# Kernel optimization log

Hardware: AMD Instinct MI355X
Metric: run time of the kernel (lower is better)

The kernel has to match this reference:

```python
import jax, jax.numpy as jnp
import numpy as np

N_ATOMS = 16384
M_NBR = 32  # neighbors per center


def setup_inputs() -> dict:
    key = jax.random.key(0)
    k1, k2, k3 = jax.random.split(key, 3)
    # atom positions in a 10 A box so a realistic fraction of pairs fall inside cutoffs
    coords = jax.random.uniform(k1, (N_ATOMS, 3), jnp.float32) * 10.0
    centers = jnp.arange(N_ATOMS, dtype=jnp.int32)
    # neighbors distinct from the center: center + offset in [1, N) mod N
    off = jax.random.randint(k2, (N_ATOMS, M_NBR), 1, N_ATOMS, dtype=jnp.int32)
    nbrs = (centers[:, None] + off) % N_ATOMS
    nl = jnp.concatenate([centers[:, None], nbrs], axis=1)  # [N, M+1]
    elements = jax.random.randint(k3, (N_ATOMS, M_NBR + 1), 0, 2, dtype=jnp.int32)
    # Stillinger-Weber parameters from __init__ (indexed by elem-sum)
    A = jnp.array([3.9781804791, 11.3797414404, 1.1907355764], jnp.float32)
    B = jnp.array([0.4446021306, 0.5266688197, 0.9015152673], jnp.float32)
    p = jnp.array([5.0, 5.0, 5.0], jnp.float32)
    q = jnp.array([0.0, 0.0, 0.0], jnp.float32)
    sigma = jnp.array([2.85295, 2.17517, 2.84133], jnp.float32)
    gamma = jnp.array([1.3566322033, 1.3566322033, 1.3566322033], jnp.float32)
    cutoff = jnp.array([5.5466, 4.02692, 4.51956], jnp.float32)
    lam = jnp.array([7.4767529158, 8.159518122], jnp.float32)
    cos_beta0 = jnp.array([0.1428569579923222, 0.1428569579923222], jnp.float32)
    cutoff_jk = jnp.array([3.86095, 5.5466], jnp.float32)
    return dict(coords=coords, A=A, B=B, p=p, q=q, sigma=sigma, gamma=gamma,
                cutoff=cutoff, lam=lam, cos_beta0=cos_beta0, cutoff_jk=cutoff_jk,
                elements=elements, nl=nl)


def reference(coords, A, B, p, q, sigma, gamma, cutoff, lam, cos_beta0, cutoff_jk, elements, nl):
    ci = nl[:, 0]            # [N] center atom indices
    nj = nl[:, 1:]           # [N, M] neighbor indices
    xi = coords[ci][:, None, :]       # [N,1,3]
    dij = coords[nj] - xi             # [N,M,3]
    rij = jnp.sqrt(jnp.sum(dij * dij, -1))  # [N,M]
    ei = elements[:, 0:1]             # [N,1]
    ej = elements[:, 1:]              # [N,M]

    # ---- two-body term ----
    s2 = ei + ej                      # in {0,1,2}
    A2, B2, p2, q2 = A[s2], B[s2], p[s2], q[s2]
    sg2, c2 = sigma[s2], cutoff[s2]
    m2 = rij < c2
    r2 = jnp.where(m2, rij, 0.5 * c2)  # safe value for masked lanes
    sr = sg2 / r2
    E2 = A2 * (B2 * sr ** p2 - sr ** q2) * jnp.exp(sg2 / (r2 - c2))
    e_pair = 0.5 * jnp.sum(jnp.where(m2, E2, 0.0))

    # ---- three-body term over all j<k neighbor pairs per center ----
    Mn = rij.shape[1]
    jj, kk = np.triu_indices(Mn, 1)   # static triplet enumeration, T = M(M-1)/2
    rij_t, rik_t = rij[:, jj], rij[:, kk]            # [N,T]
    djk = dij[:, kk, :] - dij[:, jj, :]
    rjk_t = jnp.sqrt(jnp.sum(djk * djk, -1))
    ej_t, ek_t = ej[:, jj], ej[:, kk]
    cond = (ei != ej_t) & (ej_t == ek_t)
    ijk = jnp.clip(2 - (ei + ej_t + ek_t), 0, 1)     # index into 2-entry lists
    gij, cij = gamma[ei + ej_t], cutoff[ei + ej_t]
    gik, cik = gamma[ei + ek_t], cutoff[ei + ek_t]
    cjk = cutoff_jk[ijk]
    m3 = cond & (rij_t < cij) & (rik_t < cik) & (rjk_t < cjk)
    rij_s = jnp.where(rij_t < cij, rij_t, 0.5 * cij)
    rik_s = jnp.where(rik_t < cik, rik_t, 0.5 * cik)
    cosb = (rij_s ** 2 + rik_s ** 2 - rjk_t ** 2) / (2.0 * rij_s * rik_s)
    E3 = lam[ijk] * jnp.exp(gij / (rij_s - cij) + gik / (rik_s - cik)) * (cosb - cos_beta0[ijk]) ** 2
    e_trip = jnp.sum(jnp.where(m3, E3, 0.0))

    return e_pair + e_trip
```

## Files before the change

### kernel.cpp

```cpp
#include <hip/hip_runtime.h>
#include <cmath>

#define NATOMS 16384
#define MNBR   32
#define ROW    33
#define APB    8

__device__ __forceinline__ float sel3(int s, float v0, float v1, float v2) {
    float r = (s == 0) ? v0 : v1;
    return (s == 2) ? v2 : r;
}

__global__ __launch_bounds__(256) void sw_energy_kernel(
    const float* __restrict__ coords,
    const float* __restrict__ A_,    const float* __restrict__ B_,
    const float* __restrict__ p_,    const float* __restrict__ q_,
    const float* __restrict__ sigma_,const float* __restrict__ gamma_,
    const float* __restrict__ cutoff_,const float* __restrict__ lam_,
    const float* __restrict__ cb0_,  const float* __restrict__ cjk_,
    const int*   __restrict__ elements,
    const int*   __restrict__ nl,
    float* __restrict__ block_sums)
{
    __shared__ float cdx[4][2][32], cdy[4][2][32], cdz[4][2][32];
    __shared__ float crr[4][2][32], chh[4][2][32];
    __shared__ float wsum[4];

    const int tid  = threadIdx.x;
    const int wave = tid >> 6;
    const int lane = tid & 63;
    const int side = lane >> 5;
    const int hl   = lane & 31;

    const float a0 = A_[0],     a1 = A_[1],     a2 = A_[2];
    const float b0 = B_[0],     b1 = B_[1],     b2 = B_[2];
    const float p0 = p_[0],     p1 = p_[1],     p2 = p_[2];
    const float q0 = q_[0],     q1 = q_[1],     q2 = q_[2];
    const float s0 = sigma_[0], s1 = sigma_[1], s2v = sigma_[2];
    const float g0 = gamma_[0], g1 = gamma_[1], g2 = gamma_[2];
    const float c0 = cutoff_[0],c1 = cutoff_[1],c2 = cutoff_[2];
    const float lam0 = lam_[0], lam1 = lam_[1];
    const float cb0v = cb0_[0], cb1v = cb0_[1];
    const float cjk0 = cjk_[0], cjk1 = cjk_[1];

    const int atom = blockIdx.x * APB + wave * 2 + side;
    const int base = atom * ROW;

    const int   ei  = elements[base];
    const int   ci  = nl[base];
    const float xix = coords[3*ci+0];
    const float xiy = coords[3*ci+1];
    const float xiz = coords[3*ci+2];

    float acc = 0.0f;

    const int   j  = nl[base + 1 + hl];
    const int   ej = elements[base + 1 + hl];
    const float dx = coords[3*j+0] - xix;
    const float dy = coords[3*j+1] - xiy;
    const float dz = coords[3*j+2] - xiz;
    const float r  = sqrtf(dx*dx + dy*dy + dz*dz);
    const int   s  = ei + ej;
    const float c  = sel3(s, c0, c1, c2);
    const bool  valid = (r < c);

    float h = 0.0f;
    if (valid) {
        const float sg     = sel3(s, s0, s1, s2v);
        const float inv_rc = 1.0f / (r - c);
        const float l2     = log2f(sg / r);
        const float e2     = sel3(s, a0, a1, a2)
                           * (sel3(s, b0, b1, b2) * exp2f(sel3(s, p0, p1, p2) * l2)
                              - exp2f(sel3(s, q0, q1, q2) * l2))
                           * expf(sg * inv_rc);
        acc += 0.5f * e2;
        h = sel3(s, g0, g1, g2) * inv_rc;
    }

    const bool participate = valid && (ej != ei);
    const unsigned long long ballot   = __ballot(participate);
    const unsigned long long halfmask = side ? 0xFFFFFFFF00000000ull : 0x00000000FFFFFFFFull;
    const int m = __popcll(ballot & halfmask);
    if (participate) {
        const int slot = __popcll(ballot & halfmask & ((1ull << lane) - 1ull));
        cdx[wave][side][slot] = dx;
        cdy[wave][side][slot] = dy;
        cdz[wave][side][slot] = dz;
        crr[wave][side][slot] = r;
        chh[wave][side][slot] = h;
    }

    const float lam_e = ei ? lam1 : lam0;
    const float cb_e  = ei ? cb1v : cb0v;
    const float cjk_e = ei ? cjk1 : cjk0;
    const float cjk2  = cjk_e * cjk_e;
    const int npairs  = (m * (m - 1)) >> 1;

    for (int t = hl; t < npairs; t += 32) {
        int kk = (int)(0.5f * (1.0f + sqrtf(8.0f * (float)t + 1.0f)));
        if (kk*(kk-1)/2 > t)          --kk;
        else if ((kk+1)*kk/2 <= t)    ++kk;
        const int jj = t - ((kk*(kk-1)) >> 1);

        const float dxv  = cdx[wave][side][kk] - cdx[wave][side][jj];
        const float dyv  = cdy[wave][side][kk] - cdy[wave][side][jj];
        const float dzv  = cdz[wave][side][kk] - cdz[wave][side][jj];
        const float rjk2 = dxv*dxv + dyv*dyv + dzv*dzv;
        if (rjk2 < cjk2) {
            const float rj   = crr[wave][side][jj];
            const float rk   = crr[wave][side][kk];
            const float cosb = (rj*rj + rk*rk - rjk2) * 0.5f / (rj * rk);
            const float dcb  = cosb - cb_e;
            acc += lam_e * expf(chh[wave][side][jj] + chh[wave][side][kk]) * dcb * dcb;
        }
    }

    #pragma unroll
    for (int off = 32; off > 0; off >>= 1)
        acc += __shfl_xor(acc, off, 64);
    if (lane == 0) wsum[wave] = acc;
    __syncthreads();
    if (tid == 0)
        block_sums[blockIdx.x] = wsum[0] + wsum[1] + wsum[2] + wsum[3];
}

__global__ __launch_bounds__(256) void sw_reduce_kernel(
    const float* __restrict__ in, float* __restrict__ out, int n)
{
    __shared__ float wsum[4];
    float acc = 0.0f;
    for (int i = threadIdx.x; i < n; i += 256) acc += in[i];
    #pragma unroll
    for (int off = 32; off > 0; off >>= 1)
        acc += __shfl_xor(acc, off, 64);
    if ((threadIdx.x & 63) == 0) wsum[threadIdx.x >> 6] = acc;
    __syncthreads();
    if (threadIdx.x == 0) out[0] = wsum[0] + wsum[1] + wsum[2] + wsum[3];
}

extern "C" void kernel_launch(void* const* d_in, const int* in_sizes, int n_in,
                              void* d_out, int out_size, void* d_ws, size_t ws_size,
                              hipStream_t stream)
{
    const float* coords  = (const float*)d_in[0];
    const float* A_      = (const float*)d_in[1];
    const float* B_      = (const float*)d_in[2];
    const float* p_      = (const float*)d_in[3];
    const float* q_      = (const float*)d_in[4];
    const float* sigma_  = (const float*)d_in[5];
    const float* gamma_  = (const float*)d_in[6];
    const float* cutoff_ = (const float*)d_in[7];
    const float* lam_    = (const float*)d_in[8];
    const float* cb0_    = (const float*)d_in[9];
    const float* cjk_    = (const float*)d_in[10];
    const int*   elements= (const int*)d_in[11];
    const int*   nl      = (const int*)d_in[12];

    float* out   = (float*)d_out;
    float* bsums = (float*)d_ws;

    const int nblocks = NATOMS / APB;
    sw_energy_kernel<<<nblocks, 256, 0, stream>>>(
        coords, A_, B_, p_, q_, sigma_, gamma_, cutoff_,
        lam_, cb0_, cjk_, elements, nl, bsums);
    sw_reduce_kernel<<<1, 256, 0, stream>>>(bsums, out, nblocks);
}
```

Before: 13.38 us.

## Pack neighbor data as float4, use fast math intrinsics, drop block barrier

Stores neighbor dx,dy,dz,r as a single float4 in shared memory so each triplet lookup is one vector LDS read instead of four scalar reads. Replaces sqrtf and divisions with the AMDGCN hardware sqrt and rcp intrinsics. Removes the shared-memory block reduction and __syncthreads by writing one partial sum per wave. The final reduce kernel then reads four times as many partials, using vectorized float4 loads in a fully unrolled loop. The approximate rcp and sqrt slightly change precision.

```diff
diff --git a/kernel.cpp b/kernel.cpp
--- a/kernel.cpp
+++ b/kernel.cpp
@@ -4,7 +4,8 @@
 #define NATOMS 16384
 #define MNBR   32
 #define ROW    33
-#define APB    8
+#define NBLK   2048
+#define NWAVESUM (NBLK * 4)
 
 __device__ __forceinline__ float sel3(int s, float v0, float v1, float v2) {
     float r = (s == 0) ? v0 : v1;
@@ -20,11 +21,10 @@
     const float* __restrict__ cb0_,  const float* __restrict__ cjk_,
     const int*   __restrict__ elements,
     const int*   __restrict__ nl,
-    float* __restrict__ block_sums)
+    float* __restrict__ wave_sums)
 {
-    __shared__ float cdx[4][2][32], cdy[4][2][32], cdz[4][2][32];
-    __shared__ float crr[4][2][32], chh[4][2][32];
-    __shared__ float wsum[4];
+    __shared__ float4 cpos[4][2][32];
+    __shared__ float  chh [4][2][32];
 
     const int tid  = threadIdx.x;
     const int wave = tid >> 6;
@@ -43,7 +43,7 @@
     const float cb0v = cb0_[0], cb1v = cb0_[1];
     const float cjk0 = cjk_[0], cjk1 = cjk_[1];
 
-    const int atom = blockIdx.x * APB + wave * 2 + side;
+    const int atom = (blockIdx.x << 3) + wave * 2 + side;
     const int base = atom * ROW;
 
     const int   ei  = elements[base];
@@ -59,7 +59,7 @@
     const float dx = coords[3*j+0] - xix;
     const float dy = coords[3*j+1] - xiy;
     const float dz = coords[3*j+2] - xiz;
-    const float r  = sqrtf(dx*dx + dy*dy + dz*dz);
+    const float r  = __builtin_amdgcn_sqrtf(dx*dx + dy*dy + dz*dz);
     const int   s  = ei + ej;
     const float c  = sel3(s, c0, c1, c2);
     const bool  valid = (r < c);
@@ -67,8 +67,8 @@
     float h = 0.0f;
     if (valid) {
         const float sg     = sel3(s, s0, s1, s2v);
-        const float inv_rc = 1.0f / (r - c);
-        const float l2     = log2f(sg / r);
+        const float inv_rc = __builtin_amdgcn_rcpf(r - c);
+        const float l2     = log2f(sg * __builtin_amdgcn_rcpf(r));
         const float e2     = sel3(s, a0, a1, a2)
                            * (sel3(s, b0, b1, b2) * exp2f(sel3(s, p0, p1, p2) * l2)
                               - exp2f(sel3(s, q0, q1, q2) * l2))
@@ -83,11 +83,8 @@
     const int m = __popcll(ballot & halfmask);
     if (participate) {
         const int slot = __popcll(ballot & halfmask & ((1ull << lane) - 1ull));
-        cdx[wave][side][slot] = dx;
-        cdy[wave][side][slot] = dy;
-        cdz[wave][side][slot] = dz;
-        crr[wave][side][slot] = r;
-        chh[wave][side][slot] = h;
+        cpos[wave][side][slot] = make_float4(dx, dy, dz, r);
+        chh [wave][side][slot] = h;
     }
 
     const float lam_e = ei ? lam1 : lam0;
@@ -97,19 +94,22 @@
     const int npairs  = (m * (m - 1)) >> 1;
 
     for (int t = hl; t < npairs; t += 32) {
-        int kk = (int)(0.5f * (1.0f + sqrtf(8.0f * (float)t + 1.0f)));
+        int kk = (int)(0.5f * (1.0f + __builtin_amdgcn_sqrtf(8.0f * (float)t + 1.0f)));
         if (kk*(kk-1)/2 > t)          --kk;
         else if ((kk+1)*kk/2 <= t)    ++kk;
         const int jj = t - ((kk*(kk-1)) >> 1);
 
-        const float dxv  = cdx[wave][side][kk] - cdx[wave][side][jj];
-        const float dyv  = cdy[wave][side][kk] - cdy[wave][side][jj];
-        const float dzv  = cdz[wave][side][kk] - cdz[wave][side][jj];
+        const float4 pj = cpos[wave][side][jj];
+        const float4 pk = cpos[wave][side][kk];
+        const float dxv  = pk.x - pj.x;
+        const float dyv  = pk.y - pj.y;
+        const float dzv  = pk.z - pj.z;
         const float rjk2 = dxv*dxv + dyv*dyv + dzv*dzv;
         if (rjk2 < cjk2) {
-            const float rj   = crr[wave][side][jj];
-            const float rk   = crr[wave][side][kk];
-            const float cosb = (rj*rj + rk*rk - rjk2) * 0.5f / (rj * rk);
+            const float rj   = pj.w;
+            const float rk   = pk.w;
+            const float cosb = (rj*rj + rk*rk - rjk2)
+                             * 0.5f * __builtin_amdgcn_rcpf(rj * rk);
             const float dcb  = cosb - cb_e;
             acc += lam_e * expf(chh[wave][side][jj] + chh[wave][side][kk]) * dcb * dcb;
         }
@@ -118,18 +118,21 @@
     #pragma unroll
     for (int off = 32; off > 0; off >>= 1)
         acc += __shfl_xor(acc, off, 64);
-    if (lane == 0) wsum[wave] = acc;
-    __syncthreads();
-    if (tid == 0)
-        block_sums[blockIdx.x] = wsum[0] + wsum[1] + wsum[2] + wsum[3];
+    if (lane == 0)
+        wave_sums[(blockIdx.x << 2) + wave] = acc;
 }
 
 __global__ __launch_bounds__(256) void sw_reduce_kernel(
-    const float* __restrict__ in, float* __restrict__ out, int n)
+    const float* __restrict__ in, float* __restrict__ out)
 {
     __shared__ float wsum[4];
+    const float4* v = (const float4*)in;
     float acc = 0.0f;
-    for (int i = threadIdx.x; i < n; i += 256) acc += in[i];
+    #pragma unroll
+    for (int i = 0; i < (NWAVESUM / 4) / 256; ++i) {
+        const float4 x = v[threadIdx.x + i * 256];
+        acc += (x.x + x.y) + (x.z + x.w);
+    }
     #pragma unroll
     for (int off = 32; off > 0; off >>= 1)
         acc += __shfl_xor(acc, off, 64);
@@ -157,11 +160,10 @@
     const int*   nl      = (const int*)d_in[12];
 
     float* out   = (float*)d_out;
-    float* bsums = (float*)d_ws;
+    float* wsums = (float*)d_ws;
 
-    const int nblocks = NATOMS / APB;
-    sw_energy_kernel<<<nblocks, 256, 0, stream>>>(
+    sw_energy_kernel<<<NBLK, 256, 0, stream>>>(
         coords, A_, B_, p_, q_, sigma_, gamma_, cutoff_,
-        lam_, cb0_, cjk_, elements, nl, bsums);
-    sw_reduce_kernel<<<1, 256, 0, stream>>>(bsums, out, nblocks);
+        lam_, cb0_, cjk_, elements, nl, wsums);
+    sw_reduce_kernel<<<1, 256, 0, stream>>>(wsums, out);
 }
```

After: 11.80 us. 1.13x faster.
